# Performance work log

Hardware: AMD Instinct MI355X
Metric: run time of the kernel (lower is better)

The kernel has to match this reference:

```python
import jax, jax.numpy as jnp
import numpy as np
import math

B, S, D, H, L, V, MAXLEN = 4, 2047, 256, 8, 2, 32000, 2048
DK = D // H
DFF = 2 * D
EPS = 1e-5


def make_pe(max_len, d):
    pos = jnp.arange(max_len, dtype=jnp.float32)[:, None]
    div = jnp.exp(jnp.arange(0, d, 2, dtype=jnp.float32) * (-math.log(10000.0) / d))
    pe = jnp.zeros((max_len, d), dtype=jnp.float32)
    pe = pe.at[:, 0::2].set(jnp.sin(pos * div))
    pe = pe.at[:, 1::2].set(jnp.cos(pos * div))
    return pe[None]  # [1, max_len, d]


def setup_inputs() -> dict:
    key = jax.random.key(0)
    ks = jax.random.split(key, 16)
    s = 0.02
    T = S + 1
    return {
        "embeddings": jax.random.normal(ks[0], (B, D), jnp.float32),
        "output_tokens": jax.random.randint(ks[1], (B, S), 0, V, jnp.int64),
        "causal_mask": jnp.tril(jnp.ones((T, T), jnp.int32))[None, None],  # [1,1,T,T]
        "key_padding_mask": jnp.ones((B, 1, 1, T), jnp.int32),
        "tok_emb": jax.random.normal(ks[2], (V, D), jnp.float32) * s,
        "pe": make_pe(MAXLEN, D),
        "Wq": jax.random.normal(ks[3], (L, D, D), jnp.float32) * s,
        "Wk": jax.random.normal(ks[4], (L, D, D), jnp.float32) * s,
        "Wv": jax.random.normal(ks[5], (L, D, D), jnp.float32) * s,
        "Wo": jax.random.normal(ks[6], (L, D, D), jnp.float32) * s,
        "bo": jnp.zeros((L, D), jnp.float32),
        "ln1_g": jnp.ones((L, D), jnp.float32),
        "ln1_b": jnp.zeros((L, D), jnp.float32),
        "W1": jax.random.normal(ks[7], (L, D, DFF), jnp.float32) * s,
        "b1": jnp.zeros((L, DFF), jnp.float32),
        "W2": jax.random.normal(ks[8], (L, DFF, D), jnp.float32) * s,
        "b2": jnp.zeros((L, D), jnp.float32),
        "ln2_g": jnp.ones((L, D), jnp.float32),
        "ln2_b": jnp.zeros((L, D), jnp.float32),
    }


def layer_norm(x, g, b):
    mu = jnp.mean(x, axis=-1, keepdims=True)
    var = jnp.mean(jnp.square(x - mu), axis=-1, keepdims=True)
    return (x - mu) * jax.lax.rsqrt(var + EPS) * g + b


def attention(x, Wq, Wk, Wv, Wo, bo, causal_mask, key_padding_mask):
    b, t, d = x.shape
    q = (x @ Wq).reshape(b, t, H, DK)
    k = (x @ Wk).reshape(b, t, H, DK)
    v = (x @ Wv).reshape(b, t, H, DK)
    scores = jnp.einsum('bqhd,bkhd->bhqk', q, k) / math.sqrt(DK)  # [B,H,T,T]
    neg = jnp.float32(-jnp.inf)
    scores = jnp.where(causal_mask == 0, neg, scores)
    scores = jnp.where(key_padding_mask == 0, neg, scores)
    attn = jax.nn.softmax(scores, axis=-1)
    out = jnp.einsum('bhqk,bkhd->bqhd', attn, v).reshape(b, t, d)
    return out @ Wo + bo


def reference(embeddings, output_tokens, causal_mask, key_padding_mask,
              tok_emb, pe, Wq, Wk, Wv, Wo, bo, ln1_g, ln1_b,
              W1, b1, W2, b2, ln2_g, ln2_b):
    emb_tok = tok_emb[output_tokens]                       # [B,S,D]
    x = jnp.concatenate([embeddings[:, None, :], emb_tok], axis=1)  # [B,T,D]
    x = x + pe[:, :x.shape[1]]
    for l in range(L):
        a = attention(x, Wq[l], Wk[l], Wv[l], Wo[l], bo[l], causal_mask, key_padding_mask)
        x = layer_norm(x + a, ln1_g[l], ln1_b[l])
        ff = jax.nn.relu(x @ W1[l] + b1[l]) @ W2[l] + b2[l]
        x = layer_norm(x + ff, ln2_g[l], ln2_b[l])
    return x[:, 1:, :]  # drop the prepended embedding position
```

## Files before the change

### kernel.cpp

```cpp
#include <hip/hip_runtime.h>
#include <cstdint>
#include <cstddef>

#define B_   4
#define S_   2047
#define T_   2048
#define D_   256
#define H_   8
#define DK_  32
#define DFF_ 512
#define L_   2

typedef short          s8v  __attribute__((ext_vector_type(8)));
typedef float          f4v  __attribute__((ext_vector_type(4)));
typedef unsigned short u4v  __attribute__((ext_vector_type(4)));
typedef unsigned short u8v  __attribute__((ext_vector_type(8)));
typedef unsigned int   u2v  __attribute__((ext_vector_type(2)));
typedef unsigned int   uint32;

union U8 { u8v v; unsigned short e[8]; };

__device__ __forceinline__ float bf2f(unsigned short h) {
    unsigned int u = ((unsigned int)h) << 16;
    float f; __builtin_memcpy(&f, &u, 4); return f;
}
__device__ __forceinline__ unsigned short f2bf(float f) {
    unsigned int u; __builtin_memcpy(&u, &f, 4);
    u += 0x7fffu + ((u >> 16) & 1u);
    return (unsigned short)(u >> 16);
}
__device__ __forceinline__ uint32 pack_bf2(float lo, float hi) {
    uint32 a, b;
    __builtin_memcpy(&a, &lo, 4); __builtin_memcpy(&b, &hi, 4);
    a += 0x8000u; b += 0x8000u;
    return __builtin_amdgcn_perm(b, a, 0x07060302);
}

#define QSCALE2 0.25503485951542068f

__global__ __launch_bounds__(256) void prep_k(
    const float* __restrict__ emb, const int* __restrict__ toks,
    const float* __restrict__ tokE, const float* __restrict__ pe,
    unsigned short* __restrict__ X,
    const float* __restrict__ Wq, const float* __restrict__ Wk,
    const float* __restrict__ Wv, const float* __restrict__ Wo,
    const float* __restrict__ W1, const float* __restrict__ W2,
    unsigned short* __restrict__ WqkvT, unsigned short* __restrict__ WoT,
    unsigned short* __restrict__ W1T, unsigned short* __restrict__ W2T)
{
    __shared__ float tile[32][33];
    if (blockIdx.x < 1024) {
        int idx = blockIdx.x * 256 + threadIdx.x;
        int d8 = (idx & 31) * 8;
        int t  = (idx >> 5) & (T_ - 1);
        int b  = idx >> 16;
        const float* src = (t == 0) ? (emb + b * D_)
                                    : (tokE + (size_t)toks[b * S_ + t - 1] * D_);
        const float* p = pe + (size_t)t * D_ + d8;
        U8 o;
#pragma unroll
        for (int j = 0; j < 8; ++j) o.e[j] = f2bf(src[d8 + j] + p[j]);
        *(u8v*)(X + (size_t)(b * T_ + t) * D_ + d8) = o.v;
        return;
    }
    int idx = blockIdx.x - 1024;
    const float* src; unsigned short* dst; int R, C, tr, tc;
    if (idx < 512) {
        int w = idx >> 7, rem = idx & 127, l = rem >> 6, t = rem & 63;
        tr = t >> 3; tc = t & 7; R = 256; C = 256;
        src = (w == 0 ? Wq : w == 1 ? Wk : w == 2 ? Wv : Wo) + (size_t)l * 65536;
        dst = (w < 3) ? WqkvT + (size_t)l * 196608 + (size_t)w * 65536
                      : WoT + (size_t)l * 65536;
    } else if (idx < 768) {
        int rem = idx - 512, l = rem >> 7, t = rem & 127;
        tr = t >> 4; tc = t & 15; R = 256; C = 512;
        src = W1 + (size_t)l * 131072; dst = W1T + (size_t)l * 131072;
    } else {
        int rem = idx - 768, l = rem >> 7, t = rem & 127;
        tr = t >> 3; tc = t & 7; R = 512; C = 256;
        src = W2 + (size_t)l * 131072; dst = W2T + (size_t)l * 131072;
    }
    int x = threadIdx.x & 31, y = threadIdx.x >> 5;
    int r0 = tr * 32, c0 = tc * 32;
#pragma unroll
    for (int i = 0; i < 32; i += 8) tile[y + i][x] = src[(size_t)(r0 + y + i) * C + c0 + x];
    __syncthreads();
#pragma unroll
    for (int i = 0; i < 32; i += 8)
        dst[(size_t)(c0 + y + i) * R + r0 + x] = f2bf(tile[x][y + i]);
}

__global__ __launch_bounds__(256) void gemm64_k(
    const unsigned short* __restrict__ A, const unsigned short* __restrict__ WT,
    const float* __restrict__ bias,
    unsigned short* __restrict__ oq, unsigned short* __restrict__ ok,
    unsigned short* __restrict__ ov, unsigned short* __restrict__ out,
    int K, int Ntot, int mode)
{
    __shared__ unsigned short At[64 * 72];
    __shared__ unsigned short Wt[64 * 72];
    const int tid = threadIdx.x;
    const int wave = tid >> 6, lane = tid & 63, l15 = lane & 15, quad = lane >> 4;
    const int m0 = blockIdx.x * 64, n0g = blockIdx.y * 64;

    f4v acc[4];
#pragma unroll
    for (int i = 0; i < 4; ++i) acc[i] = (f4v){0.f, 0.f, 0.f, 0.f};

    const int arow = tid >> 2, acg = (tid & 3) * 16;
    const unsigned short* ag = A + (size_t)(m0 + arow) * K + acg;
    const unsigned short* wg = WT + (size_t)(n0g + arow) * K + acg;
    u8v a0 = *(const u8v*)ag, a1 = *(const u8v*)(ag + 8);
    u8v w0 = *(const u8v*)wg, w1 = *(const u8v*)(wg + 8);

    const int niter = K >> 6;
    for (int kk = 0; kk < niter; ++kk) {
        *(u8v*)&At[arow * 72 + acg] = a0; *(u8v*)&At[arow * 72 + acg + 8] = a1;
        *(u8v*)&Wt[arow * 72 + acg] = w0; *(u8v*)&Wt[arow * 72 + acg + 8] = w1;
        __syncthreads();
        if (kk + 1 < niter) {
            int o = (kk + 1) * 64;
            a0 = *(const u8v*)(ag + o); a1 = *(const u8v*)(ag + o + 8);
            w0 = *(const u8v*)(wg + o); w1 = *(const u8v*)(wg + o + 8);
        }
#pragma unroll
        for (int ks = 0; ks < 2; ++ks) {
            s8v aF = *(const s8v*)&At[(wave * 16 + l15) * 72 + ks * 32 + quad * 8];
#pragma unroll
            for (int nt = 0; nt < 4; ++nt) {
                s8v wF = *(const s8v*)&Wt[(nt * 16 + l15) * 72 + ks * 32 + quad * 8];
                acc[nt] = __builtin_amdgcn_mfma_f32_16x16x32_bf16(aF, wF, acc[nt], 0, 0, 0);
            }
        }
        __syncthreads();
    }

    const int b = m0 >> 11, t0 = m0 & (T_ - 1);
    if (mode == 0) {
        int sub = blockIdx.y >> 2;
        int cb  = (blockIdx.y & 3) * 64;
        if (sub < 2) {
            unsigned short* dst = sub ? ok : oq;
            float sc = sub ? 1.f : QSCALE2;
#pragma unroll
            for (int nt = 0; nt < 4; ++nt) {
                int c = cb + nt * 16 + l15, hh = c >> 5, dk = c & 31;
#pragma unroll
                for (int r = 0; r < 4; ++r) {
                    int t = t0 + wave * 16 + quad * 4 + r;
                    dst[((size_t)(b * H_ + hh) * T_ + t) * DK_ + dk] = f2bf(acc[nt][r] * sc);
                }
            }
        } else {
            unsigned short* Vb = At;
#pragma unroll
            for (int nt = 0; nt < 4; ++nt) {
                int base = (nt * 16 + l15) * 72 + wave * 16 + quad * 4;
                *(uint32*)&Vb[base]     = pack_bf2(acc[nt][0], acc[nt][1]);
                *(uint32*)&Vb[base + 2] = pack_bf2(acc[nt][2], acc[nt][3]);
            }
            __syncthreads();
            int c = tid >> 2, chunk = tid & 3;
            int cg = cb + c, hh = cg >> 5, dk = cg & 31;
            unsigned short* dst = ov + ((size_t)(b * H_ + hh) * DK_ + dk) * T_ + t0 + chunk * 16;
            u8v v0 = *(u8v*)&Vb[c * 72 + chunk * 16];
            u8v v1 = *(u8v*)&Vb[c * 72 + chunk * 16 + 8];
            *(u8v*)dst = v0; *(u8v*)(dst + 8) = v1;
        }
    } else {
#pragma unroll
        for (int nt = 0; nt < 4; ++nt) {
            int c = n0g + nt * 16 + l15;
            float bv = bias[c];
#pragma unroll
            for (int r = 0; r < 4; ++r) {
                float v = acc[nt][r] + bv;
                v = v > 0.f ? v : 0.f;
                out[(size_t)(m0 + wave * 16 + quad * 4 + r) * Ntot + c] = f2bf(v);
            }
        }
    }
}

__global__ __launch_bounds__(512) void tail32_k(
    const unsigned short* __restrict__ AO,
    const unsigned short* __restrict__ WoTl, const float* __restrict__ bo,
    const unsigned short* __restrict__ Xres,
    const float* __restrict__ g1, const float* __restrict__ be1,
    const unsigned short* __restrict__ W1Tl, const float* __restrict__ b1,
    const unsigned short* __restrict__ W2Tl, const float* __restrict__ b2,
    const float* __restrict__ g2, const float* __restrict__ be2,
    unsigned short* __restrict__ Xout, float* __restrict__ fout, int last)
{
    __shared__ unsigned short Wt[256 * 72];
    __shared__ unsigned short As[32 * 72];
    __shared__ unsigned short X1s[32 * 264];
    __shared__ unsigned short Hs[32 * 520];
    __shared__ float LNsc[256];

    const int tid = threadIdx.x;
    const int wave = tid >> 6, lane = tid & 63, l15 = lane & 15, quad = lane >> 4;
    const int wr = wave >> 2, wc = wave & 3;
    const int m0 = blockIdx.x * 32;
    const int rbase = wr * 16 + quad * 4;

    const int wrow = tid >> 1, wcol = (tid & 1) * 32;
    const int arow = tid >> 3, acol = (tid & 7) * 8;

    f4v acc[4];
    u8v w0, w1, w2, w3, a0 = {0,0,0,0,0,0,0,0};

    const unsigned short* wgo = WoTl + (size_t)wrow * 256 + wcol;
    const unsigned short* wg1 = W1Tl + (size_t)wrow * 256 + wcol;
    const unsigned short* wg1b = W1Tl + (size_t)(256 + wrow) * 256 + wcol;
    const unsigned short* wg2 = W2Tl + (size_t)wrow * 512 + wcol;
    const unsigned short* ag  = AO + (size_t)(m0 + arow) * 256 + acol;

#define LDW(p, o) { w0 = *(const u8v*)((p)+(o)); w1 = *(const u8v*)((p)+(o)+8); \
                    w2 = *(const u8v*)((p)+(o)+16); w3 = *(const u8v*)((p)+(o)+24); }
#define STW { *(u8v*)&Wt[wrow*72+wcol] = w0; *(u8v*)&Wt[wrow*72+wcol+8] = w1; \
              *(u8v*)&Wt[wrow*72+wcol+16] = w2; *(u8v*)&Wt[wrow*72+wcol+24] = w3; }

#pragma unroll
    for (int i = 0; i < 4; ++i) acc[i] = (f4v){0.f, 0.f, 0.f, 0.f};
    LDW(wgo, 0);
    if (tid < 256) a0 = *(const u8v*)ag;
    for (int kk = 0; kk < 4; ++kk) {
        STW;
        if (tid < 256) *(u8v*)&As[arow * 72 + acol] = a0;
        __syncthreads();
        if (kk < 3) {
            LDW(wgo, (kk + 1) * 64);
            if (tid < 256) a0 = *(const u8v*)(ag + (kk + 1) * 64);
        } else {
            LDW(wg1, 0);
        }
#pragma unroll
        for (int ks = 0; ks < 2; ++ks) {
            s8v aF = *(const s8v*)&As[(wr * 16 + l15) * 72 + ks * 32 + quad * 8];
#pragma unroll
            for (int nt = 0; nt < 4; ++nt) {
                s8v wF = *(const s8v*)&Wt[(wc * 64 + nt * 16 + l15) * 72 + ks * 32 + quad * 8];
                acc[nt] = __builtin_amdgcn_mfma_f32_16x16x32_bf16(aF, wF, acc[nt], 0, 0, 0);
            }
        }
        __syncthreads();
    }
    {
        float ps[4] = {0,0,0,0}, pq[4] = {0,0,0,0};
#pragma unroll
        for (int nt = 0; nt < 4; ++nt) {
            int c = wc * 64 + nt * 16 + l15;
            float bv = bo[c];
#pragma unroll
            for (int r = 0; r < 4; ++r) {
                float v = acc[nt][r] + bv + bf2f(Xres[(size_t)(m0 + rbase + r) * D_ + c]);
                acc[nt][r] = v; ps[r] += v; pq[r] += v * v;
            }
        }
#pragma unroll
        for (int r = 0; r < 4; ++r) {
            float s = ps[r], q = pq[r];
            s += __shfl_xor(s, 1); q += __shfl_xor(q, 1);
            s += __shfl_xor(s, 2); q += __shfl_xor(q, 2);
            s += __shfl_xor(s, 4); q += __shfl_xor(q, 4);
            s += __shfl_xor(s, 8); q += __shfl_xor(q, 8);
            if (l15 == 0) { LNsc[(rbase + r) * 4 + wc] = s; LNsc[128 + (rbase + r) * 4 + wc] = q; }
        }
        __syncthreads();
#pragma unroll
        for (int r = 0; r < 4; ++r) {
            int row = rbase + r;
            float s = LNsc[row * 4] + LNsc[row * 4 + 1] + LNsc[row * 4 + 2] + LNsc[row * 4 + 3];
            float q = LNsc[128 + row * 4] + LNsc[128 + row * 4 + 1] + LNsc[128 + row * 4 + 2] + LNsc[128 + row * 4 + 3];
            float m = s * (1.f / 256.f);
            float rs = rsqrtf(q * (1.f / 256.f) - m * m + 1e-5f);
#pragma unroll
            for (int nt = 0; nt < 4; ++nt) {
                int c = wc * 64 + nt * 16 + l15;
                X1s[row * 264 + c] = f2bf((acc[nt][r] - m) * rs * g1[c] + be1[c]);
            }
        }
        __syncthreads();
    }

#pragma unroll
    for (int i = 0; i < 4; ++i) acc[i] = (f4v){0.f, 0.f, 0.f, 0.f};
    for (int kk = 0; kk < 4; ++kk) {
        STW;
        __syncthreads();
        if (kk < 3) LDW(wg1, (kk + 1) * 64) else LDW(wg1b, 0);
#pragma unroll
        for (int ks = 0; ks < 2; ++ks) {
            s8v aF = *(const s8v*)&X1s[(wr * 16 + l15) * 264 + kk * 64 + ks * 32 + quad * 8];
#pragma unroll
            for (int nt = 0; nt < 4; ++nt) {
                s8v wF = *(const s8v*)&Wt[(wc * 64 + nt * 16 + l15) * 72 + ks * 32 + quad * 8];
                acc[nt] = __builtin_amdgcn_mfma_f32_16x16x32_bf16(aF, wF, acc[nt], 0, 0, 0);
            }
        }
        __syncthreads();
    }
#pragma unroll
    for (int nt = 0; nt < 4; ++nt) {
        int c = wc * 64 + nt * 16 + l15;
        float bv = b1[c];
#pragma unroll
        for (int r = 0; r < 4; ++r) {
            float v = acc[nt][r] + bv; v = v > 0.f ? v : 0.f;
            Hs[(rbase + r) * 520 + c] = f2bf(v);
        }
    }

#pragma unroll
    for (int i = 0; i < 4; ++i) acc[i] = (f4v){0.f, 0.f, 0.f, 0.f};
    for (int kk = 0; kk < 4; ++kk) {
        STW;
        __syncthreads();
        if (kk < 3) LDW(wg1b, (kk + 1) * 64) else LDW(wg2, 0);
#pragma unroll
        for (int ks = 0; ks < 2; ++ks) {
            s8v aF = *(const s8v*)&X1s[(wr * 16 + l15) * 264 + kk * 64 + ks * 32 + quad * 8];
#pragma unroll
            for (int nt = 0; nt < 4; ++nt) {
                s8v wF = *(const s8v*)&Wt[(wc * 64 + nt * 16 + l15) * 72 + ks * 32 + quad * 8];
                acc[nt] = __builtin_amdgcn_mfma_f32_16x16x32_bf16(aF, wF, acc[nt], 0, 0, 0);
            }
        }
        __syncthreads();
    }
#pragma unroll
    for (int nt = 0; nt < 4; ++nt) {
        int c = wc * 64 + nt * 16 + l15;
        float bv = b1[256 + c];
#pragma unroll
        for (int r = 0; r < 4; ++r) {
            float v = acc[nt][r] + bv; v = v > 0.f ? v : 0.f;
            Hs[(rbase + r) * 520 + 256 + c] = f2bf(v);
        }
    }

#pragma unroll
    for (int i = 0; i < 4; ++i) acc[i] = (f4v){0.f, 0.f, 0.f, 0.f};
    for (int kk = 0; kk < 8; ++kk) {
        STW;
        __syncthreads();
        if (kk < 7) LDW(wg2, (kk + 1) * 64);
#pragma unroll
        for (int ks = 0; ks < 2; ++ks) {
            s8v aF = *(const s8v*)&Hs[(wr * 16 + l15) * 520 + kk * 64 + ks * 32 + quad * 8];
#pragma unroll
            for (int nt = 0; nt < 4; ++nt) {
                s8v wF = *(const s8v*)&Wt[(wc * 64 + nt * 16 + l15) * 72 + ks * 32 + quad * 8];
                acc[nt] = __builtin_amdgcn_mfma_f32_16x16x32_bf16(aF, wF, acc[nt], 0, 0, 0);
            }
        }
        __syncthreads();
    }
    {
        float ps[4] = {0,0,0,0}, pq[4] = {0,0,0,0};
#pragma unroll
        for (int nt = 0; nt < 4; ++nt) {
            int c = wc * 64 + nt * 16 + l15;
            float bv = b2[c];
#pragma unroll
            for (int r = 0; r < 4; ++r) {
                float v = acc[nt][r] + bv + bf2f(X1s[(rbase + r) * 264 + c]);
                acc[nt][r] = v; ps[r] += v; pq[r] += v * v;
            }
        }
#pragma unroll
        for (int r = 0; r < 4; ++r) {
            float s = ps[r], q = pq[r];
            s += __shfl_xor(s, 1); q += __shfl_xor(q, 1);
            s += __shfl_xor(s, 2); q += __shfl_xor(q, 2);
            s += __shfl_xor(s, 4); q += __shfl_xor(q, 4);
            s += __shfl_xor(s, 8); q += __shfl_xor(q, 8);
            if (l15 == 0) { LNsc[(rbase + r) * 4 + wc] = s; LNsc[128 + (rbase + r) * 4 + wc] = q; }
        }
        __syncthreads();
#pragma unroll
        for (int r = 0; r < 4; ++r) {
            int row = rbase + r;
            float s = LNsc[row * 4] + LNsc[row * 4 + 1] + LNsc[row * 4 + 2] + LNsc[row * 4 + 3];
            float q = LNsc[128 + row * 4] + LNsc[128 + row * 4 + 1] + LNsc[128 + row * 4 + 2] + LNsc[128 + row * 4 + 3];
            float m = s * (1.f / 256.f);
            float rs = rsqrtf(q * (1.f / 256.f) - m * m + 1e-5f);
#pragma unroll
            for (int nt = 0; nt < 4; ++nt) {
                int c = wc * 64 + nt * 16 + l15;
                float val = (acc[nt][r] - m) * rs * g2[c] + be2[c];
                if (!last) {
                    Xout[(size_t)(m0 + row) * D_ + c] = f2bf(val);
                } else {
                    int gr = m0 + row;
                    int t = gr & (T_ - 1), bb = gr >> 11;
                    if (t) fout[((size_t)bb * S_ + t - 1) * D_ + c] = val;
                }
            }
        }
    }
#undef LDW
#undef STW
}

#define KTP 5120
#define VTP 4864
__global__ __launch_bounds__(256) void attn_k(
    const unsigned short* __restrict__ Qh, const unsigned short* __restrict__ Kh,
    const unsigned short* __restrict__ VT, unsigned short* __restrict__ AO)
{
    __shared__ unsigned short Kt[2 * KTP];
    __shared__ unsigned short Vt[2 * VTP];
    __shared__ unsigned short Ps[4][16 * 136];

    const int tid = threadIdx.x, wave = tid >> 6, lane = tid & 63;
    const int l15 = lane & 15, quad = lane >> 4;
    const int bh = blockIdx.y, b = bh >> 3, h = bh & 7;
    const size_t hoff = (size_t)bh * T_ * DK_;
    unsigned short* Pw = &Ps[wave][0];

    const int qts[2] = { (int)blockIdx.x, 31 - (int)blockIdx.x };
    const int nk0 = qts[0] / 2 + 1, nk1 = qts[1] / 2 + 1;
    const int ntot = nk0 + nk1;

    const int krow = tid >> 1, khalf = (tid & 1) * 16;
    const int vdk = tid >> 3, vc = (tid & 7) * 16;
    const unsigned short* kgp = Kh + hoff + (size_t)krow * DK_ + khalf;
    const unsigned short* vgp = VT + ((size_t)bh * DK_ + vdk) * T_ + vc;

    u8v kr0 = *(const u8v*)kgp, kr1 = *(const u8v*)(kgp + 8);
    u8v vr0 = *(const u8v*)vgp, vr1 = *(const u8v*)(vgp + 8);

    s8v qB = {0,0,0,0,0,0,0,0};
    f4v O0 = {0,0,0,0}, O1 = {0,0,0,0};
    float l_i = 0.f;
    int nkt = 0, q0w = 0;

    for (int it = 0; it < ntot; ++it) {
        const int phase = (it >= nk0);
        const int kt = phase ? it - nk0 : it;
        unsigned short* Ktb = Kt + (it & 1) * KTP;
        unsigned short* Vtb = Vt + (it & 1) * VTP;
        if (kt == 0) {
            int qt = qts[phase]; nkt = phase ? nk1 : nk0;
            q0w = qt * 64 + wave * 16;
            qB = *(const s8v*)(Qh + hoff + (size_t)(q0w + l15) * DK_ + quad * 8);
            O0 = (f4v){0,0,0,0}; O1 = (f4v){0,0,0,0};
            l_i = 0.f;
        }
        *(u8v*)&Ktb[krow * 40 + khalf]     = kr0;
        *(u8v*)&Ktb[krow * 40 + khalf + 8] = kr1;
        *(u8v*)&Vtb[vdk * 152 + vc]        = vr0;
        *(u8v*)&Vtb[vdk * 152 + vc + 8]    = vr1;
        __syncthreads();
        {
            int itn = it + 1;
            if (itn < ntot) {
                int ktn = (itn >= nk0) ? itn - nk0 : itn;
                const unsigned short* kn = kgp + (size_t)ktn * 128 * DK_;
                const unsigned short* vn = vgp + (size_t)ktn * 128;
                kr0 = *(const u8v*)kn; kr1 = *(const u8v*)(kn + 8);
                vr0 = *(const u8v*)vn; vr1 = *(const u8v*)(vn + 8);
            }
        }
        const int k0 = kt * 128;

        f4v s[8];
        f4v zero = {0,0,0,0};
#pragma unroll
        for (int nt = 0; nt < 8; ++nt) {
            s8v kA = *(const s8v*)&Ktb[(nt * 16 + l15) * 40 + quad * 8];
            s[nt] = __builtin_amdgcn_mfma_f32_16x16x32_bf16(kA, qB, zero, 0, 0, 0);
        }
        if (kt == nkt - 1) {
            int query = q0w + l15;
#pragma unroll
            for (int nt = 0; nt < 8; ++nt)
#pragma unroll
                for (int r = 0; r < 4; ++r) {
                    int key = k0 + nt * 16 + quad * 4 + r;
                    if (key > query) s[nt][r] = -1e30f;
                }
        }
        float rs = 0.f;
#pragma unroll
        for (int nt = 0; nt < 8; ++nt)
#pragma unroll
            for (int r = 0; r < 4; ++r) {
                float p = exp2f(s[nt][r]);
                s[nt][r] = p;
                rs += p;
            }
        rs += __shfl_xor(rs, 16);
        rs += __shfl_xor(rs, 32);
        l_i += rs;
#pragma unroll
        for (int nt = 0; nt < 8; ++nt) {
            u2v pw;
            pw.x = pack_bf2(s[nt][0], s[nt][1]);
            pw.y = pack_bf2(s[nt][2], s[nt][3]);
            *(u2v*)&Pw[l15 * 136 + nt * 16 + quad * 4] = pw;
        }
#pragma unroll
        for (int ks = 0; ks < 4; ++ks) {
            s8v aP = *(const s8v*)&Pw[l15 * 136 + ks * 32 + quad * 8];
            s8v v0 = *(const s8v*)&Vtb[l15 * 152 + ks * 32 + quad * 8];
            s8v v1 = *(const s8v*)&Vtb[(16 + l15) * 152 + ks * 32 + quad * 8];
            O0 = __builtin_amdgcn_mfma_f32_16x16x32_bf16(aP, v0, O0, 0, 0, 0);
            O1 = __builtin_amdgcn_mfma_f32_16x16x32_bf16(aP, v1, O1, 0, 0, 0);
        }
        if (kt == nkt - 1) {
#pragma unroll
            for (int r = 0; r < 4; ++r) {
                float linv = 1.f / __shfl(l_i, quad * 4 + r);
                int row = q0w + quad * 4 + r;
                size_t base = (size_t)(b * T_ + row) * D_ + h * DK_;
                AO[base + l15]      = f2bf(O0[r] * linv);
                AO[base + 16 + l15] = f2bf(O1[r] * linv);
            }
        }
    }
}

extern "C" void kernel_launch(void* const* d_in, const int* in_sizes, int n_in,
                              void* d_out, int out_size, void* d_ws, size_t ws_size,
                              hipStream_t stream)
{
    const float* emb  = (const float*)d_in[0];
    const int*   toks = (const int*)d_in[1];
    const float* tokE = (const float*)d_in[4];
    const float* pe   = (const float*)d_in[5];
    const float* Wq   = (const float*)d_in[6];
    const float* Wk   = (const float*)d_in[7];
    const float* Wv   = (const float*)d_in[8];
    const float* Wo   = (const float*)d_in[9];
    const float* bo   = (const float*)d_in[10];
    const float* g1   = (const float*)d_in[11];
    const float* be1  = (const float*)d_in[12];
    const float* W1   = (const float*)d_in[13];
    const float* b1   = (const float*)d_in[14];
    const float* W2   = (const float*)d_in[15];
    const float* b2   = (const float*)d_in[16];
    const float* g2   = (const float*)d_in[17];
    const float* be2  = (const float*)d_in[18];
    float* out = (float*)d_out;

    unsigned short* ws = (unsigned short*)d_ws;
    size_t off = 0;
    const size_t XSZ = (size_t)B_ * T_ * D_;
    unsigned short* Xa    = ws + off; off += XSZ;
    unsigned short* Xb    = ws + off; off += XSZ;
    unsigned short* Qh    = ws + off; off += XSZ;
    unsigned short* Kh    = ws + off; off += XSZ;
    unsigned short* VTb   = ws + off; off += XSZ;
    unsigned short* AOb   = ws + off; off += XSZ;
    unsigned short* Hb    = ws + off; off += (size_t)B_ * T_ * DFF_;
    unsigned short* WqkvT = ws + off; off += (size_t)L_ * 3 * D_ * D_;
    unsigned short* WoT   = ws + off; off += (size_t)L_ * D_ * D_;
    unsigned short* W1T   = ws + off; off += (size_t)L_ * D_ * DFF_;
    unsigned short* W2T   = ws + off; off += (size_t)L_ * DFF_ * D_;
    (void)ws_size; (void)in_sizes; (void)n_in; (void)out_size;
    (void)Xb; (void)Hb;

    prep_k<<<dim3(2048), 256, 0, stream>>>(emb, toks, tokE, pe, Xa,
                                           Wq, Wk, Wv, Wo, W1, W2,
                                           WqkvT, WoT, W1T, W2T);

    for (int l = 0; l < L_; ++l) {
        const unsigned short* wqkv = WqkvT + (size_t)l * 3 * D_ * D_;
        const unsigned short* wo   = WoT + (size_t)l * D_ * D_;
        const unsigned short* w1   = W1T + (size_t)l * D_ * DFF_;
        const unsigned short* w2   = W2T + (size_t)l * DFF_ * D_;
        const int last = (l == L_ - 1);

        gemm64_k<<<dim3(128, 12), 256, 0, stream>>>(Xa, wqkv, nullptr,
                                                    Qh, Kh, VTb, nullptr, D_, D_, 0);
        attn_k<<<dim3(16, 32), 256, 0, stream>>>(Qh, Kh, VTb, AOb);
        tail32_k<<<dim3(256), 512, 0, stream>>>(AOb, wo, bo + l * D_, Xa,
                                                g1 + l * D_, be1 + l * D_,
                                                w1, b1 + l * DFF_,
                                                w2, b2 + l * D_,
                                                g2 + l * D_, be2 + l * D_,
                                                Xa, out, last);
    }
}
```

Before: 260.0 us.

## Double-buffer weight tiles in fused tail kernel with a single unified stage loop

Restructures the fused Wo/LN1/FFN/LN2 tail kernel into one 20-step loop over K-chunks with double-buffered shared-memory weight and activation tiles. The next tile is stored while the current one is consumed, cutting one of the two barriers per chunk and overlapping global loads two steps ahead. The cost is more LDS (two weight buffers) and branchier loop code, which may lower occupancy or raise register pressure.

```diff
diff --git a/kernel.cpp b/kernel.cpp
--- a/kernel.cpp
+++ b/kernel.cpp
@@ -13,7 +13,6 @@
 
 typedef short          s8v  __attribute__((ext_vector_type(8)));
 typedef float          f4v  __attribute__((ext_vector_type(4)));
-typedef unsigned short u4v  __attribute__((ext_vector_type(4)));
 typedef unsigned short u8v  __attribute__((ext_vector_type(8)));
 typedef unsigned int   u2v  __attribute__((ext_vector_type(2)));
 typedef unsigned int   uint32;
@@ -192,8 +191,8 @@
     const float* __restrict__ g2, const float* __restrict__ be2,
     unsigned short* __restrict__ Xout, float* __restrict__ fout, int last)
 {
-    __shared__ unsigned short Wt[256 * 72];
-    __shared__ unsigned short As[32 * 72];
+    __shared__ unsigned short Wt[2][256 * 72];
+    __shared__ unsigned short As[2][32 * 72];
     __shared__ unsigned short X1s[32 * 264];
     __shared__ unsigned short Hs[32 * 520];
     __shared__ float LNsc[256];
@@ -207,198 +206,163 @@
     const int wrow = tid >> 1, wcol = (tid & 1) * 32;
     const int arow = tid >> 3, acol = (tid & 7) * 8;
 
+    const unsigned short* wgo  = WoTl + (size_t)wrow * 256 + wcol;
+    const unsigned short* wg1  = W1Tl + (size_t)wrow * 256 + wcol;
+    const unsigned short* wg1b = W1Tl + (size_t)(256 + wrow) * 256 + wcol;
+    const unsigned short* wg2  = W2Tl + (size_t)wrow * 512 + wcol;
+    const unsigned short* ag   = AO + (size_t)(m0 + arow) * 256 + acol;
+
     f4v acc[4];
     u8v w0, w1, w2, w3, a0 = {0,0,0,0,0,0,0,0};
 
-    const unsigned short* wgo = WoTl + (size_t)wrow * 256 + wcol;
-    const unsigned short* wg1 = W1Tl + (size_t)wrow * 256 + wcol;
-    const unsigned short* wg1b = W1Tl + (size_t)(256 + wrow) * 256 + wcol;
-    const unsigned short* wg2 = W2Tl + (size_t)wrow * 512 + wcol;
-    const unsigned short* ag  = AO + (size_t)(m0 + arow) * 256 + acol;
-
 #define LDW(p, o) { w0 = *(const u8v*)((p)+(o)); w1 = *(const u8v*)((p)+(o)+8); \
                     w2 = *(const u8v*)((p)+(o)+16); w3 = *(const u8v*)((p)+(o)+24); }
-#define STW { *(u8v*)&Wt[wrow*72+wcol] = w0; *(u8v*)&Wt[wrow*72+wcol+8] = w1; \
-              *(u8v*)&Wt[wrow*72+wcol+16] = w2; *(u8v*)&Wt[wrow*72+wcol+24] = w3; }
+#define STW(bf) { *(u8v*)&Wt[bf][wrow*72+wcol] = w0; *(u8v*)&Wt[bf][wrow*72+wcol+8] = w1; \
+                  *(u8v*)&Wt[bf][wrow*72+wcol+16] = w2; *(u8v*)&Wt[bf][wrow*72+wcol+24] = w3; }
+
+    auto wptr = [&](int g) -> const unsigned short* {
+        if (g < 4)  return wgo  + g * 64;
+        if (g < 8)  return wg1  + (g - 4) * 64;
+        if (g < 12) return wg1b + (g - 8) * 64;
+        return wg2 + (g - 12) * 64;
+    };
+
+    LDW(wptr(0), 0);
+    if (tid < 256) a0 = *(const u8v*)ag;
+    STW(0);
+    if (tid < 256) *(u8v*)&As[0][arow * 72 + acol] = a0;
+    LDW(wptr(1), 0);
+    if (tid < 256) a0 = *(const u8v*)(ag + 64);
+    __syncthreads();
 
 #pragma unroll
     for (int i = 0; i < 4; ++i) acc[i] = (f4v){0.f, 0.f, 0.f, 0.f};
-    LDW(wgo, 0);
-    if (tid < 256) a0 = *(const u8v*)ag;
-    for (int kk = 0; kk < 4; ++kk) {
-        STW;
-        if (tid < 256) *(u8v*)&As[arow * 72 + acol] = a0;
-        __syncthreads();
-        if (kk < 3) {
-            LDW(wgo, (kk + 1) * 64);
-            if (tid < 256) a0 = *(const u8v*)(ag + (kk + 1) * 64);
-        } else {
-            LDW(wg1, 0);
-        }
+
+    for (int g = 0; g < 20; ++g) {
+        const int cur = g & 1, nxt = cur ^ 1;
+        if (g == 4 || g == 8 || g == 12) {
+#pragma unroll
+            for (int i = 0; i < 4; ++i) acc[i] = (f4v){0.f, 0.f, 0.f, 0.f};
+        }
+        if (g + 1 < 20) STW(nxt);
+        if (g + 1 < 4 && tid < 256) *(u8v*)&As[nxt][arow * 72 + acol] = a0;
+        if (g + 2 < 20) LDW(wptr(g + 2), 0);
+        if (g + 2 < 4 && tid < 256) a0 = *(const u8v*)(ag + (g + 2) * 64);
+
 #pragma unroll
         for (int ks = 0; ks < 2; ++ks) {
-            s8v aF = *(const s8v*)&As[(wr * 16 + l15) * 72 + ks * 32 + quad * 8];
-#pragma unroll
-            for (int nt = 0; nt < 4; ++nt) {
-                s8v wF = *(const s8v*)&Wt[(wc * 64 + nt * 16 + l15) * 72 + ks * 32 + quad * 8];
+            s8v aF;
+            if (g < 4)       aF = *(const s8v*)&As[cur][(wr * 16 + l15) * 72 + ks * 32 + quad * 8];
+            else if (g < 12) aF = *(const s8v*)&X1s[(wr * 16 + l15) * 264 + ((g - 4) & 3) * 64 + ks * 32 + quad * 8];
+            else             aF = *(const s8v*)&Hs[(wr * 16 + l15) * 520 + (g - 12) * 64 + ks * 32 + quad * 8];
+#pragma unroll
+            for (int nt = 0; nt < 4; ++nt) {
+                s8v wF = *(const s8v*)&Wt[cur][(wc * 64 + nt * 16 + l15) * 72 + ks * 32 + quad * 8];
                 acc[nt] = __builtin_amdgcn_mfma_f32_16x16x32_bf16(aF, wF, acc[nt], 0, 0, 0);
             }
         }
-        __syncthreads();
-    }
-    {
-        float ps[4] = {0,0,0,0}, pq[4] = {0,0,0,0};
-#pragma unroll
-        for (int nt = 0; nt < 4; ++nt) {
-            int c = wc * 64 + nt * 16 + l15;
-            float bv = bo[c];
-#pragma unroll
-            for (int r = 0; r < 4; ++r) {
-                float v = acc[nt][r] + bv + bf2f(Xres[(size_t)(m0 + rbase + r) * D_ + c]);
-                acc[nt][r] = v; ps[r] += v; pq[r] += v * v;
-            }
-        }
-#pragma unroll
-        for (int r = 0; r < 4; ++r) {
-            float s = ps[r], q = pq[r];
-            s += __shfl_xor(s, 1); q += __shfl_xor(q, 1);
-            s += __shfl_xor(s, 2); q += __shfl_xor(q, 2);
-            s += __shfl_xor(s, 4); q += __shfl_xor(q, 4);
-            s += __shfl_xor(s, 8); q += __shfl_xor(q, 8);
-            if (l15 == 0) { LNsc[(rbase + r) * 4 + wc] = s; LNsc[128 + (rbase + r) * 4 + wc] = q; }
-        }
-        __syncthreads();
-#pragma unroll
-        for (int r = 0; r < 4; ++r) {
-            int row = rbase + r;
-            float s = LNsc[row * 4] + LNsc[row * 4 + 1] + LNsc[row * 4 + 2] + LNsc[row * 4 + 3];
-            float q = LNsc[128 + row * 4] + LNsc[128 + row * 4 + 1] + LNsc[128 + row * 4 + 2] + LNsc[128 + row * 4 + 3];
-            float m = s * (1.f / 256.f);
-            float rs = rsqrtf(q * (1.f / 256.f) - m * m + 1e-5f);
+
+        if (g == 3) {
+            float ps[4] = {0,0,0,0}, pq[4] = {0,0,0,0};
 #pragma unroll
             for (int nt = 0; nt < 4; ++nt) {
                 int c = wc * 64 + nt * 16 + l15;
-                X1s[row * 264 + c] = f2bf((acc[nt][r] - m) * rs * g1[c] + be1[c]);
-            }
-        }
-        __syncthreads();
-    }
-
-#pragma unroll
-    for (int i = 0; i < 4; ++i) acc[i] = (f4v){0.f, 0.f, 0.f, 0.f};
-    for (int kk = 0; kk < 4; ++kk) {
-        STW;
-        __syncthreads();
-        if (kk < 3) LDW(wg1, (kk + 1) * 64) else LDW(wg1b, 0);
-#pragma unroll
-        for (int ks = 0; ks < 2; ++ks) {
-            s8v aF = *(const s8v*)&X1s[(wr * 16 + l15) * 264 + kk * 64 + ks * 32 + quad * 8];
-#pragma unroll
-            for (int nt = 0; nt < 4; ++nt) {
-                s8v wF = *(const s8v*)&Wt[(wc * 64 + nt * 16 + l15) * 72 + ks * 32 + quad * 8];
-                acc[nt] = __builtin_amdgcn_mfma_f32_16x16x32_bf16(aF, wF, acc[nt], 0, 0, 0);
-            }
-        }
-        __syncthreads();
-    }
-#pragma unroll
-    for (int nt = 0; nt < 4; ++nt) {
-        int c = wc * 64 + nt * 16 + l15;
-        float bv = b1[c];
-#pragma unroll
-        for (int r = 0; r < 4; ++r) {
-            float v = acc[nt][r] + bv; v = v > 0.f ? v : 0.f;
-            Hs[(rbase + r) * 520 + c] = f2bf(v);
-        }
-    }
-
-#pragma unroll
-    for (int i = 0; i < 4; ++i) acc[i] = (f4v){0.f, 0.f, 0.f, 0.f};
-    for (int kk = 0; kk < 4; ++kk) {
-        STW;
-        __syncthreads();
-        if (kk < 3) LDW(wg1b, (kk + 1) * 64) else LDW(wg2, 0);
-#pragma unroll
-        for (int ks = 0; ks < 2; ++ks) {
-            s8v aF = *(const s8v*)&X1s[(wr * 16 + l15) * 264 + kk * 64 + ks * 32 + quad * 8];
-#pragma unroll
-            for (int nt = 0; nt < 4; ++nt) {
-                s8v wF = *(const s8v*)&Wt[(wc * 64 + nt * 16 + l15) * 72 + ks * 32 + quad * 8];
-                acc[nt] = __builtin_amdgcn_mfma_f32_16x16x32_bf16(aF, wF, acc[nt], 0, 0, 0);
-            }
-        }
-        __syncthreads();
-    }
-#pragma unroll
-    for (int nt = 0; nt < 4; ++nt) {
-        int c = wc * 64 + nt * 16 + l15;
-        float bv = b1[256 + c];
-#pragma unroll
-        for (int r = 0; r < 4; ++r) {
-            float v = acc[nt][r] + bv; v = v > 0.f ? v : 0.f;
-            Hs[(rbase + r) * 520 + 256 + c] = f2bf(v);
-        }
-    }
-
-#pragma unroll
-    for (int i = 0; i < 4; ++i) acc[i] = (f4v){0.f, 0.f, 0.f, 0.f};
-    for (int kk = 0; kk < 8; ++kk) {
-        STW;
-        __syncthreads();
-        if (kk < 7) LDW(wg2, (kk + 1) * 64);
-#pragma unroll
-        for (int ks = 0; ks < 2; ++ks) {
-            s8v aF = *(const s8v*)&Hs[(wr * 16 + l15) * 520 + kk * 64 + ks * 32 + quad * 8];
-#pragma unroll
-            for (int nt = 0; nt < 4; ++nt) {
-                s8v wF = *(const s8v*)&Wt[(wc * 64 + nt * 16 + l15) * 72 + ks * 32 + quad * 8];
-                acc[nt] = __builtin_amdgcn_mfma_f32_16x16x32_bf16(aF, wF, acc[nt], 0, 0, 0);
-            }
-        }
-        __syncthreads();
-    }
-    {
-        float ps[4] = {0,0,0,0}, pq[4] = {0,0,0,0};
-#pragma unroll
-        for (int nt = 0; nt < 4; ++nt) {
-            int c = wc * 64 + nt * 16 + l15;
-            float bv = b2[c];
-#pragma unroll
-            for (int r = 0; r < 4; ++r) {
-                float v = acc[nt][r] + bv + bf2f(X1s[(rbase + r) * 264 + c]);
-                acc[nt][r] = v; ps[r] += v; pq[r] += v * v;
-            }
-        }
-#pragma unroll
-        for (int r = 0; r < 4; ++r) {
-            float s = ps[r], q = pq[r];
-            s += __shfl_xor(s, 1); q += __shfl_xor(q, 1);
-            s += __shfl_xor(s, 2); q += __shfl_xor(q, 2);
-            s += __shfl_xor(s, 4); q += __shfl_xor(q, 4);
-            s += __shfl_xor(s, 8); q += __shfl_xor(q, 8);
-            if (l15 == 0) { LNsc[(rbase + r) * 4 + wc] = s; LNsc[128 + (rbase + r) * 4 + wc] = q; }
-        }
-        __syncthreads();
-#pragma unroll
-        for (int r = 0; r < 4; ++r) {
-            int row = rbase + r;
-            float s = LNsc[row * 4] + LNsc[row * 4 + 1] + LNsc[row * 4 + 2] + LNsc[row * 4 + 3];
-            float q = LNsc[128 + row * 4] + LNsc[128 + row * 4 + 1] + LNsc[128 + row * 4 + 2] + LNsc[128 + row * 4 + 3];
-            float m = s * (1.f / 256.f);
-            float rs = rsqrtf(q * (1.f / 256.f) - m * m + 1e-5f);
+                float bv = bo[c];
+#pragma unroll
+                for (int r = 0; r < 4; ++r) {
+                    float v = acc[nt][r] + bv + bf2f(Xres[(size_t)(m0 + rbase + r) * D_ + c]);
+                    acc[nt][r] = v; ps[r] += v; pq[r] += v * v;
+                }
+            }
+#pragma unroll
+            for (int r = 0; r < 4; ++r) {
+                float s = ps[r], q = pq[r];
+                s += __shfl_xor(s, 1); q += __shfl_xor(q, 1);
+                s += __shfl_xor(s, 2); q += __shfl_xor(q, 2);
+                s += __shfl_xor(s, 4); q += __shfl_xor(q, 4);
+                s += __shfl_xor(s, 8); q += __shfl_xor(q, 8);
+                if (l15 == 0) { LNsc[(rbase + r) * 4 + wc] = s; LNsc[128 + (rbase + r) * 4 + wc] = q; }
+            }
+            __syncthreads();
+#pragma unroll
+            for (int r = 0; r < 4; ++r) {
+                int row = rbase + r;
+                float s = LNsc[row * 4] + LNsc[row * 4 + 1] + LNsc[row * 4 + 2] + LNsc[row * 4 + 3];
+                float q = LNsc[128 + row * 4] + LNsc[128 + row * 4 + 1] + LNsc[128 + row * 4 + 2] + LNsc[128 + row * 4 + 3];
+                float m = s * (1.f / 256.f);
+                float rsg = rsqrtf(q * (1.f / 256.f) - m * m + 1e-5f);
+#pragma unroll
+                for (int nt = 0; nt < 4; ++nt) {
+                    int c = wc * 64 + nt * 16 + l15;
+                    X1s[row * 264 + c] = f2bf((acc[nt][r] - m) * rsg * g1[c] + be1[c]);
+                }
+            }
+        } else if (g == 7) {
 #pragma unroll
             for (int nt = 0; nt < 4; ++nt) {
                 int c = wc * 64 + nt * 16 + l15;
-                float val = (acc[nt][r] - m) * rs * g2[c] + be2[c];
-                if (!last) {
-                    Xout[(size_t)(m0 + row) * D_ + c] = f2bf(val);
-                } else {
-                    int gr = m0 + row;
-                    int t = gr & (T_ - 1), bb = gr >> 11;
-                    if (t) fout[((size_t)bb * S_ + t - 1) * D_ + c] = val;
-                }
-            }
-        }
+                float bv = b1[c];
+#pragma unroll
+                for (int r = 0; r < 4; ++r) {
+                    float v = acc[nt][r] + bv; v = v > 0.f ? v : 0.f;
+                    Hs[(rbase + r) * 520 + c] = f2bf(v);
+                }
+            }
+        } else if (g == 11) {
+#pragma unroll
+            for (int nt = 0; nt < 4; ++nt) {
+                int c = wc * 64 + nt * 16 + l15;
+                float bv = b1[256 + c];
+#pragma unroll
+                for (int r = 0; r < 4; ++r) {
+                    float v = acc[nt][r] + bv; v = v > 0.f ? v : 0.f;
+                    Hs[(rbase + r) * 520 + 256 + c] = f2bf(v);
+                }
+            }
+        } else if (g == 19) {
+            float ps[4] = {0,0,0,0}, pq[4] = {0,0,0,0};
+#pragma unroll
+            for (int nt = 0; nt < 4; ++nt) {
+                int c = wc * 64 + nt * 16 + l15;
+                float bv = b2[c];
+#pragma unroll
+                for (int r = 0; r < 4; ++r) {
+                    float v = acc[nt][r] + bv + bf2f(X1s[(rbase + r) * 264 + c]);
+                    acc[nt][r] = v; ps[r] += v; pq[r] += v * v;
+                }
+            }
+#pragma unroll
+            for (int r = 0; r < 4; ++r) {
+                float s = ps[r], q = pq[r];
+                s += __shfl_xor(s, 1); q += __shfl_xor(q, 1);
+                s += __shfl_xor(s, 2); q += __shfl_xor(q, 2);
+                s += __shfl_xor(s, 4); q += __shfl_xor(q, 4);
+                s += __shfl_xor(s, 8); q += __shfl_xor(q, 8);
+                if (l15 == 0) { LNsc[(rbase + r) * 4 + wc] = s; LNsc[128 + (rbase + r) * 4 + wc] = q; }
+            }
+            __syncthreads();
+#pragma unroll
+            for (int r = 0; r < 4; ++r) {
+                int row = rbase + r;
+                float s = LNsc[row * 4] + LNsc[row * 4 + 1] + LNsc[row * 4 + 2] + LNsc[row * 4 + 3];
+                float q = LNsc[128 + row * 4] + LNsc[128 + row * 4 + 1] + LNsc[128 + row * 4 + 2] + LNsc[128 + row * 4 + 3];
+                float m = s * (1.f / 256.f);
+                float rsg = rsqrtf(q * (1.f / 256.f) - m * m + 1e-5f);
+#pragma unroll
+                for (int nt = 0; nt < 4; ++nt) {
+                    int c = wc * 64 + nt * 16 + l15;
+                    float val = (acc[nt][r] - m) * rsg * g2[c] + be2[c];
+                    if (!last) {
+                        Xout[(size_t)(m0 + row) * D_ + c] = f2bf(val);
+                    } else {
+                        int gr = m0 + row;
+                        int t = gr & (T_ - 1), bb = gr >> 11;
+                        if (t) fout[((size_t)bb * S_ + t - 1) * D_ + c] = val;
+                    }
+                }
+            }
+        }
+        if (g != 19) __syncthreads();
     }
 #undef LDW
 #undef STW
```

After: 262.7 us. About the same (+1.0%).

## Process both paired query tiles concurrently with 8 waves sharing K/V tiles

Applied to the files above, without the earlier changes.

The attention kernel previously walked its two paired query tiles (x and 31-x) one after the other with 4 waves, reloading the shared K/V tiles for each. It now launches 512 threads, with one group of 4 waves per query tile, so both groups consume the same K/V tile staged in LDS once per iteration. The shorter tile's group simply idles once its causal range ends. This cuts K/V global loads and loop iterations and adds parallelism per block, but the idle waves waste slots and the higher LDS and register pressure could limit occupancy.

```diff
diff --git a/kernel.cpp b/kernel.cpp
--- a/kernel.cpp
+++ b/kernel.cpp
@@ -13,7 +13,6 @@
 
 typedef short          s8v  __attribute__((ext_vector_type(8)));
 typedef float          f4v  __attribute__((ext_vector_type(4)));
-typedef unsigned short u4v  __attribute__((ext_vector_type(4)));
 typedef unsigned short u8v  __attribute__((ext_vector_type(8)));
 typedef unsigned int   u2v  __attribute__((ext_vector_type(2)));
 typedef unsigned int   uint32;
@@ -406,118 +405,104 @@
 
 #define KTP 5120
 #define VTP 4864
-__global__ __launch_bounds__(256) void attn_k(
+__global__ __launch_bounds__(512, 4) void attn_k(
     const unsigned short* __restrict__ Qh, const unsigned short* __restrict__ Kh,
     const unsigned short* __restrict__ VT, unsigned short* __restrict__ AO)
 {
     __shared__ unsigned short Kt[2 * KTP];
     __shared__ unsigned short Vt[2 * VTP];
-    __shared__ unsigned short Ps[4][16 * 136];
+    __shared__ unsigned short Ps[8][16 * 136];
 
     const int tid = threadIdx.x, wave = tid >> 6, lane = tid & 63;
     const int l15 = lane & 15, quad = lane >> 4;
+    const int grp = wave >> 2, wl = wave & 3;
     const int bh = blockIdx.y, b = bh >> 3, h = bh & 7;
     const size_t hoff = (size_t)bh * T_ * DK_;
     unsigned short* Pw = &Ps[wave][0];
 
-    const int qts[2] = { (int)blockIdx.x, 31 - (int)blockIdx.x };
-    const int nk0 = qts[0] / 2 + 1, nk1 = qts[1] / 2 + 1;
-    const int ntot = nk0 + nk1;
-
-    const int krow = tid >> 1, khalf = (tid & 1) * 16;
-    const int vdk = tid >> 3, vc = (tid & 7) * 16;
-    const unsigned short* kgp = Kh + hoff + (size_t)krow * DK_ + khalf;
+    const int x = blockIdx.x;
+    const int qt = grp ? 31 - x : x;
+    const int nkt = qt / 2 + 1;
+    const int nmax = (31 - x) / 2 + 1;
+
+    const int krow = tid >> 2, kcol = (tid & 3) * 8;
+    const int vdk = tid >> 4, vc = (tid & 15) * 8;
+    const unsigned short* kgp = Kh + hoff + (size_t)krow * DK_ + kcol;
     const unsigned short* vgp = VT + ((size_t)bh * DK_ + vdk) * T_ + vc;
 
-    u8v kr0 = *(const u8v*)kgp, kr1 = *(const u8v*)(kgp + 8);
-    u8v vr0 = *(const u8v*)vgp, vr1 = *(const u8v*)(vgp + 8);
-
-    s8v qB = {0,0,0,0,0,0,0,0};
+    u8v kr = *(const u8v*)kgp;
+    u8v vr = *(const u8v*)vgp;
+
+    const int q0w = qt * 64 + wl * 16;
+    const s8v qB = *(const s8v*)(Qh + hoff + (size_t)(q0w + l15) * DK_ + quad * 8);
     f4v O0 = {0,0,0,0}, O1 = {0,0,0,0};
     float l_i = 0.f;
-    int nkt = 0, q0w = 0;
-
-    for (int it = 0; it < ntot; ++it) {
-        const int phase = (it >= nk0);
-        const int kt = phase ? it - nk0 : it;
-        unsigned short* Ktb = Kt + (it & 1) * KTP;
-        unsigned short* Vtb = Vt + (it & 1) * VTP;
-        if (kt == 0) {
-            int qt = qts[phase]; nkt = phase ? nk1 : nk0;
-            q0w = qt * 64 + wave * 16;
-            qB = *(const s8v*)(Qh + hoff + (size_t)(q0w + l15) * DK_ + quad * 8);
-            O0 = (f4v){0,0,0,0}; O1 = (f4v){0,0,0,0};
-            l_i = 0.f;
-        }
-        *(u8v*)&Ktb[krow * 40 + khalf]     = kr0;
-        *(u8v*)&Ktb[krow * 40 + khalf + 8] = kr1;
-        *(u8v*)&Vtb[vdk * 152 + vc]        = vr0;
-        *(u8v*)&Vtb[vdk * 152 + vc + 8]    = vr1;
-        __syncthreads();
-        {
-            int itn = it + 1;
-            if (itn < ntot) {
-                int ktn = (itn >= nk0) ? itn - nk0 : itn;
-                const unsigned short* kn = kgp + (size_t)ktn * 128 * DK_;
-                const unsigned short* vn = vgp + (size_t)ktn * 128;
-                kr0 = *(const u8v*)kn; kr1 = *(const u8v*)(kn + 8);
-                vr0 = *(const u8v*)vn; vr1 = *(const u8v*)(vn + 8);
-            }
-        }
-        const int k0 = kt * 128;
-
-        f4v s[8];
-        f4v zero = {0,0,0,0};
-#pragma unroll
-        for (int nt = 0; nt < 8; ++nt) {
-            s8v kA = *(const s8v*)&Ktb[(nt * 16 + l15) * 40 + quad * 8];
-            s[nt] = __builtin_amdgcn_mfma_f32_16x16x32_bf16(kA, qB, zero, 0, 0, 0);
-        }
-        if (kt == nkt - 1) {
-            int query = q0w + l15;
+
+    for (int kt = 0; kt < nmax; ++kt) {
+        unsigned short* Ktb = Kt + (kt & 1) * KTP;
+        unsigned short* Vtb = Vt + (kt & 1) * VTP;
+        *(u8v*)&Ktb[krow * 40 + kcol] = kr;
+        *(u8v*)&Vtb[vdk * 152 + vc]   = vr;
+        __syncthreads();
+        if (kt + 1 < nmax) {
+            kr = *(const u8v*)(kgp + (size_t)(kt + 1) * 128 * DK_);
+            vr = *(const u8v*)(vgp + (kt + 1) * 128);
+        }
+        if (kt < nkt) {
+            const int k0 = kt * 128;
+            f4v s[8];
+            f4v zero = {0,0,0,0};
+#pragma unroll
+            for (int nt = 0; nt < 8; ++nt) {
+                s8v kA = *(const s8v*)&Ktb[(nt * 16 + l15) * 40 + quad * 8];
+                s[nt] = __builtin_amdgcn_mfma_f32_16x16x32_bf16(kA, qB, zero, 0, 0, 0);
+            }
+            if (kt == nkt - 1) {
+                int query = q0w + l15;
+#pragma unroll
+                for (int nt = 0; nt < 8; ++nt)
+#pragma unroll
+                    for (int r = 0; r < 4; ++r) {
+                        int key = k0 + nt * 16 + quad * 4 + r;
+                        if (key > query) s[nt][r] = -1e30f;
+                    }
+            }
+            float rs = 0.f;
 #pragma unroll
             for (int nt = 0; nt < 8; ++nt)
 #pragma unroll
                 for (int r = 0; r < 4; ++r) {
-                    int key = k0 + nt * 16 + quad * 4 + r;
-                    if (key > query) s[nt][r] = -1e30f;
+                    float p = exp2f(s[nt][r]);
+                    s[nt][r] = p;
+                    rs += p;
                 }
-        }
-        float rs = 0.f;
-#pragma unroll
-        for (int nt = 0; nt < 8; ++nt)
-#pragma unroll
-            for (int r = 0; r < 4; ++r) {
-                float p = exp2f(s[nt][r]);
-                s[nt][r] = p;
-                rs += p;
-            }
-        rs += __shfl_xor(rs, 16);
-        rs += __shfl_xor(rs, 32);
-        l_i += rs;
-#pragma unroll
-        for (int nt = 0; nt < 8; ++nt) {
-            u2v pw;
-            pw.x = pack_bf2(s[nt][0], s[nt][1]);
-            pw.y = pack_bf2(s[nt][2], s[nt][3]);
-            *(u2v*)&Pw[l15 * 136 + nt * 16 + quad * 4] = pw;
-        }
-#pragma unroll
-        for (int ks = 0; ks < 4; ++ks) {
-            s8v aP = *(const s8v*)&Pw[l15 * 136 + ks * 32 + quad * 8];
-            s8v v0 = *(const s8v*)&Vtb[l15 * 152 + ks * 32 + quad * 8];
-            s8v v1 = *(const s8v*)&Vtb[(16 + l15) * 152 + ks * 32 + quad * 8];
-            O0 = __builtin_amdgcn_mfma_f32_16x16x32_bf16(aP, v0, O0, 0, 0, 0);
-            O1 = __builtin_amdgcn_mfma_f32_16x16x32_bf16(aP, v1, O1, 0, 0, 0);
-        }
-        if (kt == nkt - 1) {
-#pragma unroll
-            for (int r = 0; r < 4; ++r) {
-                float linv = 1.f / __shfl(l_i, quad * 4 + r);
-                int row = q0w + quad * 4 + r;
-                size_t base = (size_t)(b * T_ + row) * D_ + h * DK_;
-                AO[base + l15]      = f2bf(O0[r] * linv);
-                AO[base + 16 + l15] = f2bf(O1[r] * linv);
+            rs += __shfl_xor(rs, 16);
+            rs += __shfl_xor(rs, 32);
+            l_i += rs;
+#pragma unroll
+            for (int nt = 0; nt < 8; ++nt) {
+                u2v pw;
+                pw.x = pack_bf2(s[nt][0], s[nt][1]);
+                pw.y = pack_bf2(s[nt][2], s[nt][3]);
+                *(u2v*)&Pw[l15 * 136 + nt * 16 + quad * 4] = pw;
+            }
+#pragma unroll
+            for (int ks = 0; ks < 4; ++ks) {
+                s8v aP = *(const s8v*)&Pw[l15 * 136 + ks * 32 + quad * 8];
+                s8v v0 = *(const s8v*)&Vtb[l15 * 152 + ks * 32 + quad * 8];
+                s8v v1 = *(const s8v*)&Vtb[(16 + l15) * 152 + ks * 32 + quad * 8];
+                O0 = __builtin_amdgcn_mfma_f32_16x16x32_bf16(aP, v0, O0, 0, 0, 0);
+                O1 = __builtin_amdgcn_mfma_f32_16x16x32_bf16(aP, v1, O1, 0, 0, 0);
+            }
+            if (kt == nkt - 1) {
+#pragma unroll
+                for (int r = 0; r < 4; ++r) {
+                    float linv = 1.f / __shfl(l_i, quad * 4 + r);
+                    int row = q0w + quad * 4 + r;
+                    size_t base = (size_t)(b * T_ + row) * D_ + h * DK_;
+                    AO[base + l15]      = f2bf(O0[r] * linv);
+                    AO[base + 16 + l15] = f2bf(O1[r] * linv);
+                }
             }
         }
     }
@@ -576,7 +561,7 @@
 
         gemm64_k<<<dim3(128, 12), 256, 0, stream>>>(Xa, wqkv, nullptr,
                                                     Qh, Kh, VTb, nullptr, D_, D_, 0);
-        attn_k<<<dim3(16, 32), 256, 0, stream>>>(Qh, Kh, VTb, AOb);
+        attn_k<<<dim3(16, 32), 512, 0, stream>>>(Qh, Kh, VTb, AOb);
         tail32_k<<<dim3(256), 512, 0, stream>>>(AOb, wo, bo + l * D_, Xa,
                                                 g1 + l * D_, be1 + l * D_,
                                                 w1, b1 + l * DFF_,
```

Result: no change. 256.2 us (-1.5%).
